# Performance work log

Hardware: AMD Instinct MI355X
Metric: run time of the kernel (lower is better)

Reference implementation:

```python
import jax, jax.numpy as jnp
import numpy as np

B, N, D, H, A = 1024, 8, 256, 512, 4  # batch, num_objects, embedding_dim, hidden_dim, action_dim


def _edge_list(batch, n):
    # Fully connected (no self-loops) over n nodes, replicated per sample with offset b*n.
    pairs = np.array([(i, j) for i in range(n) for j in range(n) if i != j], dtype=np.int32)
    off = (np.arange(batch, dtype=np.int32) * n)[:, None]
    row = (pairs[:, 0][None, :] + off).reshape(-1)
    col = (pairs[:, 1][None, :] + off).reshape(-1)
    return jnp.asarray(row), jnp.asarray(col)


def _layer_norm(x, g, b):
    m = x.mean(-1, keepdims=True)
    v = x.var(-1, keepdims=True)
    return (x - m) / jnp.sqrt(v + 1e-5) * g + b


def _mlp(x, w1, b1, w2, b2, g, bn, w3, b3):
    h = jax.nn.relu(x @ w1 + b1)
    h = jax.nn.relu(_layer_norm(h @ w2 + b2, g, bn))
    return h @ w3 + b3


def setup_inputs() -> dict:
    key = jax.random.key(0)
    ks = jax.random.split(key, 12)
    def w(k, shape):
        return jax.random.normal(k, shape, jnp.float32) / np.sqrt(shape[0]).astype(np.float32)
    return {
        "states": jax.random.normal(ks[0], (B, N, D), jnp.float32),
        "action": jax.random.randint(ks[1], (B,), 0, A),
        # edge MLP: 3D -> H -> H (LN) -> H
        "e_w1": w(ks[2], (3 * D, H)), "e_b1": jnp.zeros((H,), jnp.float32),
        "e_w2": w(ks[3], (H, H)),     "e_b2": jnp.zeros((H,), jnp.float32),
        "e_g":  jnp.ones((H,), jnp.float32), "e_bn": jnp.zeros((H,), jnp.float32),
        "e_w3": w(ks[4], (H, H)),     "e_b3": jnp.zeros((H,), jnp.float32),
        # node MLP: H + D + A -> H -> H (LN) -> D
        "n_w1": w(ks[5], (H + D + A, H)), "n_b1": jnp.zeros((H,), jnp.float32),
        "n_w2": w(ks[6], (H, H)),         "n_b2": jnp.zeros((H,), jnp.float32),
        "n_g":  jnp.ones((H,), jnp.float32), "n_bn": jnp.zeros((H,), jnp.float32),
        "n_w3": w(ks[7], (H, D)),         "n_b3": jnp.zeros((D,), jnp.float32),
    }


def reference(states, action,
              e_w1, e_b1, e_w2, e_b2, e_g, e_bn, e_w3, e_b3,
              n_w1, n_b1, n_w2, n_b2, n_g, n_bn, n_w3, n_b3):
    eP = (e_w1, e_b1, e_w2, e_b2, e_g, e_bn, e_w3, e_b3)
    nP = (n_w1, n_b1, n_w2, n_b2, n_g, n_bn, n_w3, n_b3)
    flat = states.reshape(-1, D)                       # [B*N, D]
    row, col = _edge_list(B, N - 1)                    # faithful: edge list over N-1 objects
    E = row.shape[0]
    # copy_action / embodied: one-hot action repeated per object
    av = jnp.repeat(jax.nn.one_hot(action, A, dtype=flat.dtype), N, axis=0)  # [B*N, A]
    # round 0: edge_attr starts as zeros like node features
    e = _mlp(jnp.concatenate([flat[row], jnp.zeros((E, D), flat.dtype), flat[col]], 1), *eP)
    agg = jax.ops.segment_sum(e, row, num_segments=B * N)  # [B*N, H]
    node = _mlp(jnp.concatenate([flat, av, agg], 1), *nP)   # [B*N, D]
    flat = flat + node
    av0 = jnp.zeros_like(av)
    for _ in range(N - 1):
        e = _mlp(jnp.concatenate([flat[row], node[row], flat[col]], 1), *eP)
        agg = jax.ops.segment_sum(e, row, num_segments=B * N)
        node = _mlp(jnp.concatenate([flat, av0, agg], 1), *nP)
        flat = flat + node
    return flat.reshape(B, N, D)
```

## Files before the change

### kernel.cpp

```cpp
#include <hip/hip_runtime.h>
#include <cstddef>

typedef _Float16 f16x8 __attribute__((ext_vector_type(8)));
typedef _Float16 f16x4 __attribute__((ext_vector_type(4)));
typedef float f32x16 __attribute__((ext_vector_type(16)));
typedef unsigned short ushort_t;

#define NSEG 7168
#define NNODE 8192

enum { EP_NONE = 0, EP_BIAS = 1, EP_RAWP = 2, EP_NL1 = 3, EP_NL3 = 4 };

#define PHASE_BARRIER() do { asm volatile("s_waitcnt lgkmcnt(0)" ::: "memory"); \
                             __builtin_amdgcn_s_barrier(); } while (0)

#define RELU8(v) do { _Pragma("unroll") \
  for (int j_ = 0; j_ < 8; ++j_) v[j_] = v[j_] > (_Float16)0 ? v[j_] : (_Float16)0; } while (0)

__global__ __launch_bounds__(256)
void prepack(const float* __restrict__ W, ushort_t* __restrict__ P,
             int koff, int kcnt, int N) {
  int idx = blockIdx.x * 256 + threadIdx.x;
  if (idx >= kcnt * N) return;
  int kl = idx / N, n = idx - kl * N;
  _Float16 h = (_Float16)W[idx];
  int k = koff + kl;
  int NT = N >> 5;
  size_t o = ((((size_t)(k >> 4)) * NT + (n >> 5)) * 64 + ((k >> 3) & 1) * 32 + (n & 31)) * 8 + (k & 7);
  P[o] = __builtin_bit_cast(ushort_t, h);
}

__global__ __launch_bounds__(256)
void v6k(const float* __restrict__ eb3, const float* __restrict__ nw1,
         float* __restrict__ v6) {
  int n = blockIdx.x * 256 + threadIdx.x;
  if (n >= 512) return;
  float a = 0.f;
  for (int k = 0; k < 512; ++k) a += eb3[k] * nw1[(size_t)(260 + k) * 512 + n];
  v6[n] = 6.f * a;
}

template <int NCOLB, int EPI, int EDGE, int LNIN, int X1F16, int OUTF16>
__global__ __launch_bounds__(256, 4)
void gemmT(const void* __restrict__ X1v, int ld1, int nph1,
           const void* __restrict__ X2v, int ld2, int nph2,
           const ushort_t* __restrict__ Sm, const ushort_t* __restrict__ Tm,
           const ushort_t* __restrict__ P,
           const float* __restrict__ bias, const float* __restrict__ bias2,
           const int* __restrict__ action, const float* __restrict__ wact,
           const float* __restrict__ lnmu, const float* __restrict__ lnrsd,
           const float* __restrict__ lng, const float* __restrict__ lnbn,
           void* __restrict__ Yv, float* __restrict__ Yres,
           float* __restrict__ Part, int m0base) {
  constexpr int N = NCOLB * 128;
  constexpr int NT = N / 32;
  const int u = threadIdx.x;
  const int nwg = gridDim.x;
  const int qq = nwg >> 3, r8 = nwg & 7;
  const int xcd = blockIdx.x & 7, inx = blockIdx.x >> 3;
  const int logical = (xcd < r8 ? xcd * (qq + 1) : r8 * (qq + 1) + (xcd - r8) * qq) + inx;
  const int mY = (logical / NCOLB) * 64;
  const int cb = logical - (logical / NCOLB) * NCOLB;
  const int nB = cb * 128;
  const int lane = u & 63, w = u >> 6;
  const int wr = w >> 1, wc = w & 1;
  const int r31 = lane & 31, rt2 = lane >> 5;

  __shared__ ushort_t lA[16384];
  __shared__ int eR[64], eC[64];

  if (EDGE) {
    if (u < 64) {
      int e = m0base + mY + u;
      int b = e / 42, p = e - b * 42;
      int i = p / 6, tt = p - i * 6;
      int j = tt + (tt >= i ? 1 : 0);
      eR[u] = b * 7 + i;
      eC[u] = b * 7 + j;
    }
    __syncthreads();
  }

  const int kcA = w * 2, kcB = w * 2 + 1;
  const int widx0 = (((rt2 * 8 + kcA) * 2 + 0) * 32 + (r31 ^ ((kcA & 3) << 3))) * 8;
  const int widx1 = (((rt2 * 8 + kcA) * 2 + 1) * 32 + (r31 ^ ((kcA & 3) << 3))) * 8;
  const int widx2 = (((rt2 * 8 + kcB) * 2 + 0) * 32 + (r31 ^ ((kcB & 3) << 3))) * 8;
  const int widx3 = (((rt2 * 8 + kcB) * 2 + 1) * 32 + (r31 ^ ((kcB & 3) << 3))) * 8;

  const ushort_t* sB = nullptr;
  const ushort_t* tB = nullptr;
  const float* x1f = nullptr;
  const ushort_t* x1h = nullptr;
  const ushort_t* x2h = nullptr;
  if (EDGE) {
    sB = Sm + (size_t)eR[lane] * 512 + w * 32;
    tB = Tm + (size_t)eC[lane] * 512 + w * 32;
  } else {
    if (X1F16) x1h = (const ushort_t*)X1v + (size_t)(mY + lane) * ld1 + w * 32;
    else       x1f = (const float*)X1v + (size_t)(mY + lane) * ld1 + w * 32;
    if (nph2 > 0) x2h = (const ushort_t*)X2v + (size_t)(mY + lane) * ld2 + w * 32;
  }
  float mym = 0.f, myr = 0.f;
  if (LNIN) { mym = lnmu[mY + lane]; myr = lnrsd[mY + lane]; }

  f16x8 xc0, xc1, xc2, xc3;
  auto loadx = [&](int ph) {
    if (EDGE) {
      const ushort_t* sp = sB + ph * 128;
      const ushort_t* tp = tB + ph * 128;
      f16x8 s0 = *(const f16x8*)sp,        t0 = *(const f16x8*)tp;
      f16x8 s1 = *(const f16x8*)(sp + 8),  t1 = *(const f16x8*)(tp + 8);
      f16x8 s2 = *(const f16x8*)(sp + 16), t2 = *(const f16x8*)(tp + 16);
      f16x8 s3 = *(const f16x8*)(sp + 24), t3 = *(const f16x8*)(tp + 24);
      xc0 = s0 + t0; xc1 = s1 + t1; xc2 = s2 + t2; xc3 = s3 + t3;
      RELU8(xc0); RELU8(xc1); RELU8(xc2); RELU8(xc3);
    } else if (!X1F16 && ph < nph1) {
      const float* src = x1f + ph * 128;
      float4 l0 = *(const float4*)(src +  0), h0 = *(const float4*)(src +  4);
      float4 l1 = *(const float4*)(src +  8), h1 = *(const float4*)(src + 12);
      float4 l2 = *(const float4*)(src + 16), h2 = *(const float4*)(src + 20);
      float4 l3 = *(const float4*)(src + 24), h3 = *(const float4*)(src + 28);
#define CVT8(X, lo, hi) do { X[0]=(_Float16)lo.x; X[1]=(_Float16)lo.y; \
      X[2]=(_Float16)lo.z; X[3]=(_Float16)lo.w; X[4]=(_Float16)hi.x; \
      X[5]=(_Float16)hi.y; X[6]=(_Float16)hi.z; X[7]=(_Float16)hi.w; } while (0)
      CVT8(xc0, l0, h0); CVT8(xc1, l1, h1); CVT8(xc2, l2, h2); CVT8(xc3, l3, h3);
#undef CVT8
    } else {
      const ushort_t* src = (ph < nph1) ? x1h + ph * 128 : x2h + (ph - nph1) * 128;
      xc0 = *(const f16x8*)src;
      xc1 = *(const f16x8*)(src + 8);
      xc2 = *(const f16x8*)(src + 16);
      xc3 = *(const f16x8*)(src + 24);
      if (LNIN) {
        const int kb = ph * 128 + w * 32;
#define LN8(X, OFS) do { _Pragma("unroll") for (int j_ = 0; j_ < 8; ++j_) { \
        float xx = (float)X[j_]; \
        xx = fmaxf((xx - mym) * myr * lng[kb + (OFS) + j_] + lnbn[kb + (OFS) + j_], 0.f); \
        X[j_] = (_Float16)xx; } } while (0)
        LN8(xc0, 0); LN8(xc1, 8); LN8(xc2, 16); LN8(xc3, 24);
#undef LN8
      }
    }
  };
  auto cvtwrite = [&](int b) {
    const int base = b * 8192;
    *(f16x8*)&lA[base + widx0] = xc0;
    *(f16x8*)&lA[base + widx1] = xc1;
    *(f16x8*)&lA[base + widx2] = xc2;
    *(f16x8*)&lA[base + widx3] = xc3;
  };

  f32x16 acc0, acc1;
  #pragma unroll
  for (int q = 0; q < 16; ++q) { acc0[q] = 0.f; acc1[q] = 0.f; }

  const int nph = nph1 + nph2;
  const int ntb = (nB >> 5) + wc * 2;
  const int TOT = nph * 8;

#define LOADA(S, A_) do { \
    const int aofs_ = lbase + (((wr * 8 + (S)) * 2 + rt2) * 32 + (r31 ^ (((S) & 3) << 3))) * 8; \
    A_ = *(const f16x8*)&lA[aofs_]; } while (0)

#define LOADB(G_, H0, H1) do { \
    const ushort_t* bp_ = P + (((size_t)(G_) * NT + ntb) * 64 + lane) * 8; \
    H0 = *(const f16x8*)bp_; \
    H1 = *(const f16x8*)(bp_ + 512); } while (0)

#define MFMA2(AH, H0, H1) do { \
    acc0 = __builtin_amdgcn_mfma_f32_32x32x16_f16(AH, H0, acc0, 0, 0, 0); \
    acc1 = __builtin_amdgcn_mfma_f32_32x32x16_f16(AH, H1, acc1, 0, 0, 0); } while (0)

  loadx(0);
  cvtwrite(0);
  if (nph > 1) loadx(1);
  PHASE_BARRIER();
  f16x8 be0, be1, bo0, bo1;
  LOADB(0, be0, be1);
  LOADB(1, bo0, bo1);

  #pragma unroll 1
  for (int ph = 0; ph < nph; ++ph) {
    if (ph + 1 < nph) {
      cvtwrite((ph + 1) & 1);
      if (ph + 2 < nph) loadx(ph + 2);
    }
    const int lbase = (ph & 1) * 8192;
    const int g0 = ph * 8;
    f16x8 ac, an;
    LOADA(0, ac);
    #pragma unroll
    for (int s = 0; s < 8; ++s) {
      if (s < 7) LOADA(s + 1, an);
      f16x8 h0, h1;
      if ((s & 1) == 0) {
        h0 = be0; h1 = be1;
        if (g0 + s + 2 < TOT) LOADB(g0 + s + 2, be0, be1);
      } else {
        h0 = bo0; h1 = bo1;
        if (g0 + s + 2 < TOT) LOADB(g0 + s + 2, bo0, bo1);
      }
      MFMA2(ac, h0, h1);
      if (s < 7) ac = an;
    }
    if (ph + 1 < nph) PHASE_BARRIER();
  }

  const int col0 = nB + wc * 64 + r31;
  float v[2][16];
  {
    float bc0 = (EPI == EP_NONE) ? 0.f : bias[col0];
    float bc1 = (EPI == EP_NONE) ? 0.f : bias[col0 + 32];
    #pragma unroll
    for (int q = 0; q < 16; ++q) {
      v[0][q] = acc0[q] + bc0;
      v[1][q] = acc1[q] + bc1;
    }
  }

  if (EPI == EP_NL1) {
    #pragma unroll
    for (int q = 0; q < 16; ++q) {
      int m = mY + wr * 32 + (q & 3) + 8 * (q >> 2) + 4 * rt2;
      if (m < NSEG) {
        v[0][q] += bias2[col0];
        v[1][q] += bias2[col0 + 32];
      }
      if (action != nullptr) {
        const float* wrp = wact + (size_t)(256 + action[m >> 3]) * 512;
        v[0][q] += wrp[col0];
        v[1][q] += wrp[col0 + 32];
      }
    }
    #pragma unroll
    for (int ct = 0; ct < 2; ++ct)
      #pragma unroll
      for (int q = 0; q < 16; ++q) v[ct][q] = fmaxf(v[ct][q], 0.f);
  }

  if (EPI == EP_RAWP) {
    float sv[16], qv[16];
    #pragma unroll
    for (int q = 0; q < 16; ++q) {
      sv[q] = v[0][q] + v[1][q];
      qv[q] = v[0][q] * v[0][q] + v[1][q] * v[1][q];
    }
    #pragma unroll
    for (int mm = 1; mm <= 16; mm <<= 1) {
      #pragma unroll
      for (int q = 0; q < 16; ++q) {
        sv[q] += __shfl_xor(sv[q], mm);
        qv[q] += __shfl_xor(qv[q], mm);
      }
    }
    if (r31 == 0) {
      #pragma unroll
      for (int q = 0; q < 16; ++q) {
        int m = mY + wr * 32 + (q & 3) + 8 * (q >> 2) + 4 * rt2;
        Part[(size_t)m * 16 + cb * 2 + wc] = sv[q];
        Part[(size_t)m * 16 + 8 + cb * 2 + wc] = qv[q];
      }
    }
  }

  #pragma unroll
  for (int ct = 0; ct < 2; ++ct) {
    #pragma unroll
    for (int q = 0; q < 16; ++q) {
      int m = mY + wr * 32 + (q & 3) + 8 * (q >> 2) + 4 * rt2;
      float z = v[ct][q];
      if (OUTF16)
        ((ushort_t*)Yv)[(size_t)m * N + col0 + ct * 32] =
            __builtin_bit_cast(ushort_t, (_Float16)z);
      else
        ((float*)Yv)[(size_t)m * N + col0 + ct * 32] = z;
      if (EPI == EP_NL3) Yres[(size_t)m * N + col0 + ct * 32] += z;
    }
  }
#undef LOADA
#undef LOADB
#undef MFMA2
}

__global__ __launch_bounds__(256)
void rowstats(const float* __restrict__ Part, float* __restrict__ mu,
              float* __restrict__ rsd, int M) {
  int m = blockIdx.x * 256 + threadIdx.x;
  if (m >= M) return;
  const float* p = Part + (size_t)m * 16;
  float S = 0.f, Q = 0.f;
  #pragma unroll
  for (int i = 0; i < 8; ++i) { S += p[i]; Q += p[8 + i]; }
  float mm = S * (1.f / 512.f);
  mu[m] = mm;
  rsd[m] = rsqrtf(Q * (1.f / 512.f) - mm * mm + 1e-5f);
}

__global__ __launch_bounds__(256)
void h2_sum_ln(const ushort_t* __restrict__ H2, const float* __restrict__ mu,
               const float* __restrict__ rsd, const float* __restrict__ g,
               const float* __restrict__ bn, ushort_t* __restrict__ SS, int nrows) {
  int id = blockIdx.x * 256 + threadIdx.x;
  if (id >= nrows * 128) return;
  int ln = id >> 7, c4 = (id & 127) * 4;
  float4 gv = *(const float4*)(g + c4);
  float4 bv = *(const float4*)(bn + c4);
  float a0 = 0.f, a1 = 0.f, a2 = 0.f, a3 = 0.f;
  #pragma unroll
  for (int r = 0; r < 6; ++r) {
    int row = ln * 6 + r;
    f16x4 y = *(const f16x4*)(H2 + (size_t)row * 512 + c4);
    float m = mu[row], rs = rsd[row];
    a0 += fmaxf(((float)y[0] - m) * rs * gv.x + bv.x, 0.f);
    a1 += fmaxf(((float)y[1] - m) * rs * gv.y + bv.y, 0.f);
    a2 += fmaxf(((float)y[2] - m) * rs * gv.z + bv.z, 0.f);
    a3 += fmaxf(((float)y[3] - m) * rs * gv.w + bv.w, 0.f);
  }
  f16x4 o;
  o[0] = (_Float16)a0; o[1] = (_Float16)a1; o[2] = (_Float16)a2; o[3] = (_Float16)a3;
  *(f16x4*)(SS + (size_t)ln * 512 + c4) = o;
}

extern "C" void kernel_launch(void* const* d_in, const int* in_sizes, int n_in,
                              void* d_out, int out_size, void* d_ws, size_t ws_size,
                              hipStream_t stream) {
  (void)in_sizes; (void)n_in; (void)out_size;
  const float* states = (const float*)d_in[0];
  const int* action = (const int*)d_in[1];
  const float* e_w1 = (const float*)d_in[2];
  const float* e_b1 = (const float*)d_in[3];
  const float* e_w2 = (const float*)d_in[4];
  const float* e_b2 = (const float*)d_in[5];
  const float* e_g = (const float*)d_in[6];
  const float* e_bn = (const float*)d_in[7];
  const float* e_w3 = (const float*)d_in[8];
  const float* e_b3 = (const float*)d_in[9];
  const float* n_w1 = (const float*)d_in[10];
  const float* n_b1 = (const float*)d_in[11];
  const float* n_w2 = (const float*)d_in[12];
  const float* n_b2 = (const float*)d_in[13];
  const float* n_g = (const float*)d_in[14];
  const float* n_bn = (const float*)d_in[15];
  const float* n_w3 = (const float*)d_in[16];
  const float* n_b3 = (const float*)d_in[17];

  float* flat = (float*)d_out;
  float* fp = (float*)d_ws;
  float* Mbuf = fp;  fp += 262144;
  float* v6 = fp;    fp += 512;
  float* muE = fp;   fp += 43008;
  float* rsdE = fp;  fp += 43008;
  float* muN = fp;   fp += 8192;
  float* rsdN = fp;  fp += 8192;
  float* PartE = fp; fp += 688128;
  float* PartN = fp; fp += 131072;
  ushort_t* us = (ushort_t*)fp;
  ushort_t* node = us; us += 2097152;
  ushort_t* SS = us;   us += 4194304;
  ushort_t* G = us;    us += 4194304;
  ushort_t* G2 = us;   us += 4194304;
  ushort_t* Sb = us;   us += 3670016;
  ushort_t* Tb = us;   us += 3670016;
  ushort_t* PeWab = us; us += 262144;
  ushort_t* PeWc = us;  us += 131072;
  ushort_t* PeW2 = us;  us += 262144;
  ushort_t* Ptmp = us;  us += 262144;
  ushort_t* PnW1M = us; us += 393216;
  ushort_t* PnW2 = us;  us += 262144;
  ushort_t* PnW3 = us;  us += 131072;
  ushort_t* H2 = us;

  const size_t fixedB = (size_t)((char*)H2 - (char*)d_ws);
  int nc = 32;
  for (int cand = 1; cand <= 32; cand <<= 1)
    if (fixedB + (43008ull / cand) * 512ull * 2ull <= ws_size) { nc = cand; break; }
  const int spc = 1024 / nc;
  const int epc = spc * 42;

  prepack<<<1024, 256, 0, stream>>>(e_w1, PeWab, 0, 512, 512);
  prepack<<<512, 256, 0, stream>>>(e_w1 + 262144, PeWc, 0, 256, 512);
  prepack<<<1024, 256, 0, stream>>>(e_w2, PeW2, 0, 512, 512);
  prepack<<<1024, 256, 0, stream>>>(n_w1 + 133120, Ptmp, 0, 512, 512);
  prepack<<<512, 256, 0, stream>>>(n_w1, PnW1M, 0, 256, 512);
  prepack<<<1024, 256, 0, stream>>>(n_w2, PnW2, 0, 512, 512);
  prepack<<<512, 256, 0, stream>>>(n_w3, PnW3, 0, 512, 256);
  gemmT<4, EP_NONE, 0, 0, 0, 0><<<32, 256, 0, stream>>>(
      e_w3, 512, 4, nullptr, 0, 0, nullptr, nullptr, Ptmp, nullptr, nullptr,
      nullptr, nullptr, nullptr, nullptr, nullptr, nullptr, Mbuf, nullptr, nullptr, 0);
  prepack<<<1024, 256, 0, stream>>>(Mbuf, PnW1M, 256, 512, 512);
  v6k<<<2, 256, 0, stream>>>(e_b3, n_w1, v6);
  hipMemsetAsync(SS + (size_t)NSEG * 512, 0, (size_t)(NNODE - NSEG) * 512 * 2, stream);
  hipMemcpyAsync(flat, states, (size_t)NNODE * 256 * 4, hipMemcpyDeviceToDevice, stream);

  for (int round = 0; round < 8; ++round) {
    if (round == 0)
      gemmT<4, EP_BIAS, 0, 0, 0, 1><<<448, 256, 0, stream>>>(
          flat, 256, 2, nullptr, 0, 0, nullptr, nullptr, PeWab, e_b1, nullptr,
          nullptr, nullptr, nullptr, nullptr, nullptr, nullptr, Sb, nullptr, nullptr, 0);
    else
      gemmT<4, EP_BIAS, 0, 0, 0, 1><<<448, 256, 0, stream>>>(
          flat, 256, 2, node, 256, 2, nullptr, nullptr, PeWab, e_b1, nullptr,
          nullptr, nullptr, nullptr, nullptr, nullptr, nullptr, Sb, nullptr, nullptr, 0);
    gemmT<4, EP_NONE, 0, 0, 0, 1><<<448, 256, 0, stream>>>(
        flat, 256, 2, nullptr, 0, 0, nullptr, nullptr, PeWc, nullptr, nullptr,
        nullptr, nullptr, nullptr, nullptr, nullptr, nullptr, Tb, nullptr, nullptr, 0);
    for (int ch = 0; ch < nc; ++ch) {
      gemmT<4, EP_RAWP, 1, 0, 0, 1><<<(epc / 64) * 4, 256, 0, stream>>>(
          nullptr, 0, 4, nullptr, 0, 0, Sb, Tb, PeW2, e_b2, nullptr,
          nullptr, nullptr, nullptr, nullptr, nullptr, nullptr,
          H2, nullptr, PartE, ch * epc);
      rowstats<<<(epc + 255) / 256, 256, 0, stream>>>(PartE, muE, rsdE, epc);
      h2_sum_ln<<<(spc * 7 * 128) / 256, 256, 0, stream>>>(
          H2, muE, rsdE, e_g, e_bn, SS + (size_t)ch * spc * 7 * 512, spc * 7);
    }
    gemmT<4, EP_NL1, 0, 0, 0, 1><<<512, 256, 0, stream>>>(
        flat, 256, 2, SS, 512, 4, nullptr, nullptr, PnW1M, n_b1, v6,
        (round == 0) ? action : nullptr, n_w1,
        nullptr, nullptr, nullptr, nullptr, G, nullptr, nullptr, 0);
    gemmT<4, EP_RAWP, 0, 0, 1, 1><<<512, 256, 0, stream>>>(
        G, 512, 4, nullptr, 0, 0, nullptr, nullptr, PnW2, n_b2, nullptr,
        nullptr, nullptr, nullptr, nullptr, nullptr, nullptr, G2, nullptr, PartN, 0);
    rowstats<<<32, 256, 0, stream>>>(PartN, muN, rsdN, 8192);
    gemmT<2, EP_NL3, 0, 1, 1, 1><<<256, 256, 0, stream>>>(
        G2, 512, 4, nullptr, 0, 0, nullptr, nullptr, PnW3, n_b3, nullptr,
        nullptr, nullptr, muN, rsdN, n_g, n_bn, node, flat, nullptr, 0);
  }
}
```

Before: 1.340 ms.

## Merge S/T edge projections into one GEMM and fold rowstats into consumers

Packs the two first-layer edge weight blocks into one 1024-wide weight so that S and T come from a single GEMM launch writing an interleaved STb buffer. The separate rowstats kernels are removed, and LayerNorm mean and rstd are recomputed from the partial sums inside h2_sum_ln and the LN-input GEMM. The B-operand prefetch distance in the GEMM main loop is deepened from 2 to 4 stages. Together these cut kernel launches and intermediate mu/rsd traffic, at the cost of more registers per thread and some redundant stat recomputation.

Measured after the change: 1.283 ms. 1.04x faster.

```diff
diff --git a/kernel.cpp b/kernel.cpp
--- a/kernel.cpp
+++ b/kernel.cpp
@@ -19,14 +19,13 @@
 
 __global__ __launch_bounds__(256)
 void prepack(const float* __restrict__ W, ushort_t* __restrict__ P,
-             int koff, int kcnt, int N) {
+             int koff, int kcnt, int Nsrc, int NTpack, int noff) {
   int idx = blockIdx.x * 256 + threadIdx.x;
-  if (idx >= kcnt * N) return;
-  int kl = idx / N, n = idx - kl * N;
+  if (idx >= kcnt * Nsrc) return;
+  int kl = idx / Nsrc, n = idx - kl * Nsrc + noff;
   _Float16 h = (_Float16)W[idx];
   int k = koff + kl;
-  int NT = N >> 5;
-  size_t o = ((((size_t)(k >> 4)) * NT + (n >> 5)) * 64 + ((k >> 3) & 1) * 32 + (n & 31)) * 8 + (k & 7);
+  size_t o = ((((size_t)(k >> 4)) * NTpack + (n >> 5)) * 64 + ((k >> 3) & 1) * 32 + (n & 31)) * 8 + (k & 7);
   P[o] = __builtin_bit_cast(ushort_t, h);
 }
 
@@ -48,7 +47,7 @@
            const ushort_t* __restrict__ P,
            const float* __restrict__ bias, const float* __restrict__ bias2,
            const int* __restrict__ action, const float* __restrict__ wact,
-           const float* __restrict__ lnmu, const float* __restrict__ lnrsd,
+           const float* __restrict__ lnpart,
            const float* __restrict__ lng, const float* __restrict__ lnbn,
            void* __restrict__ Yv, float* __restrict__ Yres,
            float* __restrict__ Part, int m0base) {
@@ -93,15 +92,22 @@
   const ushort_t* x1h = nullptr;
   const ushort_t* x2h = nullptr;
   if (EDGE) {
-    sB = Sm + (size_t)eR[lane] * 512 + w * 32;
-    tB = Tm + (size_t)eC[lane] * 512 + w * 32;
+    sB = Sm + (size_t)eR[lane] * 1024 + w * 32;
+    tB = Tm + (size_t)eC[lane] * 1024 + w * 32;
   } else {
     if (X1F16) x1h = (const ushort_t*)X1v + (size_t)(mY + lane) * ld1 + w * 32;
     else       x1f = (const float*)X1v + (size_t)(mY + lane) * ld1 + w * 32;
     if (nph2 > 0) x2h = (const ushort_t*)X2v + (size_t)(mY + lane) * ld2 + w * 32;
   }
   float mym = 0.f, myr = 0.f;
-  if (LNIN) { mym = lnmu[mY + lane]; myr = lnrsd[mY + lane]; }
+  if (LNIN) {
+    const float* pp = lnpart + (size_t)(mY + lane) * 16;
+    float S_ = 0.f, Q_ = 0.f;
+    #pragma unroll
+    for (int i = 0; i < 8; ++i) { S_ += pp[i]; Q_ += pp[8 + i]; }
+    mym = S_ * (1.f / 512.f);
+    myr = rsqrtf(Q_ * (1.f / 512.f) - mym * mym + 1e-5f);
+  }
 
   f16x8 xc0, xc1, xc2, xc3;
   auto loadx = [&](int ph) {
@@ -175,9 +181,11 @@
   cvtwrite(0);
   if (nph > 1) loadx(1);
   PHASE_BARRIER();
-  f16x8 be0, be1, bo0, bo1;
-  LOADB(0, be0, be1);
-  LOADB(1, bo0, bo1);
+  f16x8 b00, b01, b10, b11, b20, b21, b30, b31;
+  LOADB(0, b00, b01);
+  LOADB(1, b10, b11);
+  LOADB(2, b20, b21);
+  LOADB(3, b30, b31);
 
   #pragma unroll 1
   for (int ph = 0; ph < nph; ++ph) {
@@ -189,20 +197,21 @@
     const int g0 = ph * 8;
     f16x8 ac, an;
     LOADA(0, ac);
-    #pragma unroll
-    for (int s = 0; s < 8; ++s) {
-      if (s < 7) LOADA(s + 1, an);
-      f16x8 h0, h1;
-      if ((s & 1) == 0) {
-        h0 = be0; h1 = be1;
-        if (g0 + s + 2 < TOT) LOADB(g0 + s + 2, be0, be1);
-      } else {
-        h0 = bo0; h1 = bo1;
-        if (g0 + s + 2 < TOT) LOADB(g0 + s + 2, bo0, bo1);
-      }
-      MFMA2(ac, h0, h1);
-      if (s < 7) ac = an;
-    }
+#define STEP(S, BH, BL) do { \
+    if ((S) < 7) LOADA((S) + 1, an); \
+    f16x8 h0 = BH, h1 = BL; \
+    if (g0 + (S) + 4 < TOT) LOADB(g0 + (S) + 4, BH, BL); \
+    MFMA2(ac, h0, h1); \
+    if ((S) < 7) ac = an; } while (0)
+    STEP(0, b00, b01);
+    STEP(1, b10, b11);
+    STEP(2, b20, b21);
+    STEP(3, b30, b31);
+    STEP(4, b00, b01);
+    STEP(5, b10, b11);
+    STEP(6, b20, b21);
+    STEP(7, b30, b31);
+#undef STEP
     if (ph + 1 < nph) PHASE_BARRIER();
   }
 
@@ -283,26 +292,25 @@
 }
 
 __global__ __launch_bounds__(256)
-void rowstats(const float* __restrict__ Part, float* __restrict__ mu,
-              float* __restrict__ rsd, int M) {
-  int m = blockIdx.x * 256 + threadIdx.x;
-  if (m >= M) return;
-  const float* p = Part + (size_t)m * 16;
-  float S = 0.f, Q = 0.f;
-  #pragma unroll
-  for (int i = 0; i < 8; ++i) { S += p[i]; Q += p[8 + i]; }
-  float mm = S * (1.f / 512.f);
-  mu[m] = mm;
-  rsd[m] = rsqrtf(Q * (1.f / 512.f) - mm * mm + 1e-5f);
-}
-
-__global__ __launch_bounds__(256)
-void h2_sum_ln(const ushort_t* __restrict__ H2, const float* __restrict__ mu,
-               const float* __restrict__ rsd, const float* __restrict__ g,
-               const float* __restrict__ bn, ushort_t* __restrict__ SS, int nrows) {
-  int id = blockIdx.x * 256 + threadIdx.x;
-  if (id >= nrows * 128) return;
-  int ln = id >> 7, c4 = (id & 127) * 4;
+void h2_sum_ln(const ushort_t* __restrict__ H2, const float* __restrict__ Part,
+               const float* __restrict__ g, const float* __restrict__ bn,
+               ushort_t* __restrict__ SS) {
+  __shared__ float smu[12], srs[12];
+  const int u = threadIdx.x;
+  const int g2 = blockIdx.x * 2;
+  if (u < 12) {
+    const float* pp = Part + ((size_t)g2 * 6 + u) * 16;
+    float S = 0.f, Q = 0.f;
+    #pragma unroll
+    for (int i = 0; i < 8; ++i) { S += pp[i]; Q += pp[8 + i]; }
+    float m = S * (1.f / 512.f);
+    smu[u] = m;
+    srs[u] = rsqrtf(Q * (1.f / 512.f) - m * m + 1e-5f);
+  }
+  __syncthreads();
+  const int ln = g2 + (u >> 7);
+  const int lloc = (u >> 7) * 6;
+  const int c4 = (u & 127) * 4;
   float4 gv = *(const float4*)(g + c4);
   float4 bv = *(const float4*)(bn + c4);
   float a0 = 0.f, a1 = 0.f, a2 = 0.f, a3 = 0.f;
@@ -310,7 +318,7 @@
   for (int r = 0; r < 6; ++r) {
     int row = ln * 6 + r;
     f16x4 y = *(const f16x4*)(H2 + (size_t)row * 512 + c4);
-    float m = mu[row], rs = rsd[row];
+    float m = smu[lloc + r], rs = srs[lloc + r];
     a0 += fmaxf(((float)y[0] - m) * rs * gv.x + bv.x, 0.f);
     a1 += fmaxf(((float)y[1] - m) * rs * gv.y + bv.y, 0.f);
     a2 += fmaxf(((float)y[2] - m) * rs * gv.z + bv.z, 0.f);
@@ -348,10 +356,7 @@
   float* fp = (float*)d_ws;
   float* Mbuf = fp;  fp += 262144;
   float* v6 = fp;    fp += 512;
-  float* muE = fp;   fp += 43008;
-  float* rsdE = fp;  fp += 43008;
-  float* muN = fp;   fp += 8192;
-  float* rsdN = fp;  fp += 8192;
+  float* b1ext = fp; fp += 1024;
   float* PartE = fp; fp += 688128;
   float* PartN = fp; fp += 131072;
   ushort_t* us = (ushort_t*)fp;
@@ -359,12 +364,10 @@
   ushort_t* SS = us;   us += 4194304;
   ushort_t* G = us;    us += 4194304;
   ushort_t* G2 = us;   us += 4194304;
-  ushort_t* Sb = us;   us += 3670016;
-  ushort_t* Tb = us;   us += 3670016;
-  ushort_t* PeWab = us; us += 262144;
-  ushort_t* PeWc = us;  us += 131072;
-  ushort_t* PeW2 = us;  us += 262144;
-  ushort_t* Ptmp = us;  us += 262144;
+  ushort_t* STb = us;  us += 7340032;
+  ushort_t* PeST = us; us += 524288;
+  ushort_t* PeW2 = us; us += 262144;
+  ushort_t* Ptmp = us; us += 262144;
   ushort_t* PnW1M = us; us += 393216;
   ushort_t* PnW2 = us;  us += 262144;
   ushort_t* PnW3 = us;  us += 131072;
@@ -377,52 +380,50 @@
   const int spc = 1024 / nc;
   const int epc = spc * 42;
 
-  prepack<<<1024, 256, 0, stream>>>(e_w1, PeWab, 0, 512, 512);
-  prepack<<<512, 256, 0, stream>>>(e_w1 + 262144, PeWc, 0, 256, 512);
-  prepack<<<1024, 256, 0, stream>>>(e_w2, PeW2, 0, 512, 512);
-  prepack<<<1024, 256, 0, stream>>>(n_w1 + 133120, Ptmp, 0, 512, 512);
-  prepack<<<512, 256, 0, stream>>>(n_w1, PnW1M, 0, 256, 512);
-  prepack<<<1024, 256, 0, stream>>>(n_w2, PnW2, 0, 512, 512);
-  prepack<<<512, 256, 0, stream>>>(n_w3, PnW3, 0, 512, 256);
+  hipMemsetAsync(PeST, 0, 524288 * 2, stream);
+  prepack<<<1024, 256, 0, stream>>>(e_w1, PeST, 0, 512, 512, 32, 0);
+  prepack<<<512, 256, 0, stream>>>(e_w1 + 262144, PeST, 0, 256, 512, 32, 512);
+  prepack<<<1024, 256, 0, stream>>>(e_w2, PeW2, 0, 512, 512, 16, 0);
+  prepack<<<1024, 256, 0, stream>>>(n_w1 + 133120, Ptmp, 0, 512, 512, 16, 0);
+  prepack<<<512, 256, 0, stream>>>(n_w1, PnW1M, 0, 256, 512, 16, 0);
+  prepack<<<1024, 256, 0, stream>>>(n_w2, PnW2, 0, 512, 512, 16, 0);
+  prepack<<<512, 256, 0, stream>>>(n_w3, PnW3, 0, 512, 256, 8, 0);
+  hipMemcpyAsync(b1ext, e_b1, 512 * 4, hipMemcpyDeviceToDevice, stream);
+  hipMemsetAsync(b1ext + 512, 0, 512 * 4, stream);
   gemmT<4, EP_NONE, 0, 0, 0, 0><<<32, 256, 0, stream>>>(
       e_w3, 512, 4, nullptr, 0, 0, nullptr, nullptr, Ptmp, nullptr, nullptr,
-      nullptr, nullptr, nullptr, nullptr, nullptr, nullptr, Mbuf, nullptr, nullptr, 0);
-  prepack<<<1024, 256, 0, stream>>>(Mbuf, PnW1M, 256, 512, 512);
+      nullptr, nullptr, nullptr, nullptr, nullptr, Mbuf, nullptr, nullptr, 0);
+  prepack<<<1024, 256, 0, stream>>>(Mbuf, PnW1M, 256, 512, 512, 16, 0);
   v6k<<<2, 256, 0, stream>>>(e_b3, n_w1, v6);
   hipMemsetAsync(SS + (size_t)NSEG * 512, 0, (size_t)(NNODE - NSEG) * 512 * 2, stream);
   hipMemcpyAsync(flat, states, (size_t)NNODE * 256 * 4, hipMemcpyDeviceToDevice, stream);
 
   for (int round = 0; round < 8; ++round) {
     if (round == 0)
-      gemmT<4, EP_BIAS, 0, 0, 0, 1><<<448, 256, 0, stream>>>(
-          flat, 256, 2, nullptr, 0, 0, nullptr, nullptr, PeWab, e_b1, nullptr,
-          nullptr, nullptr, nullptr, nullptr, nullptr, nullptr, Sb, nullptr, nullptr, 0);
+      gemmT<8, EP_BIAS, 0, 0, 0, 1><<<896, 256, 0, stream>>>(
+          flat, 256, 2, nullptr, 0, 0, nullptr, nullptr, PeST, b1ext, nullptr,
+          nullptr, nullptr, nullptr, nullptr, nullptr, STb, nullptr, nullptr, 0);
     else
-      gemmT<4, EP_BIAS, 0, 0, 0, 1><<<448, 256, 0, stream>>>(
-          flat, 256, 2, node, 256, 2, nullptr, nullptr, PeWab, e_b1, nullptr,
-          nullptr, nullptr, nullptr, nullptr, nullptr, nullptr, Sb, nullptr, nullptr, 0);
-    gemmT<4, EP_NONE, 0, 0, 0, 1><<<448, 256, 0, stream>>>(
-        flat, 256, 2, nullptr, 0, 0, nullptr, nullptr, PeWc, nullptr, nullptr,
-        nullptr, nullptr, nullptr, nullptr, nullptr, nullptr, Tb, nullptr, nullptr, 0);
+      gemmT<8, EP_BIAS, 0, 0, 0, 1><<<896, 256, 0, stream>>>(
+          flat, 256, 2, node, 256, 2, nullptr, nullptr, PeST, b1ext, nullptr,
+          nullptr, nullptr, nullptr, nullptr, nullptr, STb, nullptr, nullptr, 0);
     for (int ch = 0; ch < nc; ++ch) {
       gemmT<4, EP_RAWP, 1, 0, 0, 1><<<(epc / 64) * 4, 256, 0, stream>>>(
-          nullptr, 0, 4, nullptr, 0, 0, Sb, Tb, PeW2, e_b2, nullptr,
-          nullptr, nullptr, nullptr, nullptr, nullptr, nullptr,
+          nullptr, 0, 4, nullptr, 0, 0, STb, STb + 512, PeW2, e_b2, nullptr,
+          nullptr, nullptr, nullptr, nullptr, nullptr,
           H2, nullptr, PartE, ch * epc);
-      rowstats<<<(epc + 255) / 256, 256, 0, stream>>>(PartE, muE, rsdE, epc);
-      h2_sum_ln<<<(spc * 7 * 128) / 256, 256, 0, stream>>>(
-          H2, muE, rsdE, e_g, e_bn, SS + (size_t)ch * spc * 7 * 512, spc * 7);
+      h2_sum_ln<<<(spc * 7) / 2, 256, 0, stream>>>(
+          H2, PartE, e_g, e_bn, SS + (size_t)ch * spc * 7 * 512);
     }
     gemmT<4, EP_NL1, 0, 0, 0, 1><<<512, 256, 0, stream>>>(
         flat, 256, 2, SS, 512, 4, nullptr, nullptr, PnW1M, n_b1, v6,
         (round == 0) ? action : nullptr, n_w1,
-        nullptr, nullptr, nullptr, nullptr, G, nullptr, nullptr, 0);
+        nullptr, nullptr, nullptr, G, nullptr, nullptr, 0);
     gemmT<4, EP_RAWP, 0, 0, 1, 1><<<512, 256, 0, stream>>>(
         G, 512, 4, nullptr, 0, 0, nullptr, nullptr, PnW2, n_b2, nullptr,
-        nullptr, nullptr, nullptr, nullptr, nullptr, nullptr, G2, nullptr, PartN, 0);
-    rowstats<<<32, 256, 0, stream>>>(PartN, muN, rsdN, 8192);
+        nullptr, nullptr, nullptr, nullptr, nullptr, G2, nullptr, PartN, 0);
     gemmT<2, EP_NL3, 0, 1, 1, 1><<<256, 256, 0, stream>>>(
         G2, 512, 4, nullptr, 0, 0, nullptr, nullptr, PnW3, n_b3, nullptr,
-        nullptr, nullptr, muN, rsdN, n_g, n_bn, node, flat, nullptr, 0);
+        nullptr, nullptr, PartN, n_g, n_bn, node, flat, nullptr, 0);
   }
 }
```
